# Kernel tuning notes

Hardware: AMD Instinct MI355X
Metric: run time of the kernel (lower is better)

Reference implementation:

```python
import jax, jax.numpy as jnp
import numpy as np

REL_DIM = 1024
NUM_HEADS = 16
HEAD_DIM = REL_DIM // NUM_HEADS
REL_EMB_DIM = 256
B, K = 32, 512
SCALE = 1.0 / float(np.sqrt(HEAD_DIM))


def setup_inputs() -> dict:
    key = jax.random.key(0)
    ks = jax.random.split(key, 7)
    s = 1.0 / float(np.sqrt(REL_DIM))
    return {
        "h_R": jax.random.normal(ks[0], (B, K, REL_DIM), dtype=jnp.float32),
        "R": jax.random.normal(ks[1], (K, REL_EMB_DIM), dtype=jnp.float32),
        "W_q": jax.random.normal(ks[2], (REL_DIM, REL_DIM), dtype=jnp.float32) * s,
        "W_k": jax.random.normal(ks[3], (REL_DIM, REL_DIM), dtype=jnp.float32) * s,
        "W_v": jax.random.normal(ks[4], (REL_DIM, REL_DIM), dtype=jnp.float32) * s,
        "W_o": jax.random.normal(ks[5], (REL_DIM, REL_DIM), dtype=jnp.float32) * s,
        "w_sim": jax.random.normal(ks[6], (NUM_HEADS,), dtype=jnp.float32) * 0.1,
    }


def reference(h_R, R, W_q, W_k, W_v, W_o, w_sim):
    Bb, Kk, _ = h_R.shape
    H, D = NUM_HEADS, HEAD_DIM
    # torch Linear: x @ W.T ; then split heads -> (B, H, K, D)
    def proj(x, W):
        return jnp.einsum('bkd,ed->bke', x, W).reshape(Bb, Kk, H, D).transpose(0, 2, 1, 3)
    q = proj(h_R, W_q)
    k = proj(h_R, W_k)
    v = proj(h_R, W_v)
    attn = jnp.einsum('bhqd,bhkd->bhqk', q, k) * SCALE
    # cosine-similarity bias (batch-independent): (H, K, K)
    R_norm = R / jnp.maximum(jnp.linalg.norm(R, axis=-1, keepdims=True), 1e-12)
    sim = R_norm @ R_norm.T  # (K, K)
    bias = w_sim[:, None, None] * sim[None]  # (H, K, K)
    attn = attn + bias[None]
    alpha = jax.nn.softmax(attn, axis=-1)
    out = jnp.einsum('bhqk,bhkd->bhqd', alpha, v)
    out = out.transpose(0, 2, 1, 3).reshape(Bb, Kk, H * D)
    return jnp.einsum('bkd,ed->bke', out, W_o)
```

## Files before the change

kernel.cpp:

```cpp
#include <hip/hip_runtime.h>

#define SEQK 512
#define NH 16
#define HD 64
#define RD 1024
#define BBATCH 32
#define QK_SCALE 0.125f
#define LOG2E 1.4426950408889634f

typedef unsigned short u16;
typedef unsigned int u32;
using bf16x8 = __attribute__((ext_vector_type(8))) short;
using f32x4  = __attribute__((ext_vector_type(4))) float;
using f32x16 = __attribute__((ext_vector_type(16))) float;

__device__ __forceinline__ u16 f2bf(float f) {
  unsigned u = __float_as_uint(f);
  u += 0x7FFFu + ((u >> 16) & 1u);
  return (u16)(u >> 16);
}
__device__ __forceinline__ float bf2f(u16 v) {
  return __uint_as_float(((unsigned)v) << 16);
}
__device__ __forceinline__ float fexp2(float x) {
  float r;
  asm("v_exp_f32 %0, %1" : "=v"(r) : "v"(x));
  return r;
}
__device__ __forceinline__ u32 pkbf(float lo, float hi) {
  u32 r;
  asm("v_cvt_pk_bf16_f32 %0, %1, %2" : "=v"(r) : "v"(lo), "v"(hi));
  return r;
}
__device__ __forceinline__ void plswap(u32& a, u32& b) {
#if __has_builtin(__builtin_amdgcn_permlane32_swap)
  typedef int v2i __attribute__((ext_vector_type(2)));
  v2i r = __builtin_amdgcn_permlane32_swap((int)a, (int)b, false, false);
  a = (u32)r[0]; b = (u32)r[1];
#else
  asm volatile("v_permlane32_swap_b32 %0, %1" : "+v"(a), "+v"(b));
#endif
}

__device__ __forceinline__ void async_cp16(const void* g, void* l) {
  __builtin_amdgcn_global_load_lds(
      (__attribute__((address_space(1))) void*)(void*)g,
      (__attribute__((address_space(3))) void*)l,
      16, 0, 0);
}

__global__ void convert_kernel(const float* __restrict__ hR,
                               const float* __restrict__ Wq, const float* __restrict__ Wk,
                               const float* __restrict__ Wv, const float* __restrict__ Wo,
                               u16* __restrict__ hR16,
                               u16* __restrict__ Wq16, u16* __restrict__ Wk16,
                               u16* __restrict__ Wv16, u16* __restrict__ Wo16) {
  size_t i4 = (size_t)blockIdx.x * blockDim.x + threadIdx.x;
  size_t e = i4 * 4;
  const float* src; u16* dst; size_t off;
  if (e < 16777216u) { src = hR; dst = hR16; off = e; }
  else {
    size_t r = e - 16777216u;
    int w = (int)(r >> 20);
    off = r & 1048575u;
    src = (w == 0 ? Wq : w == 1 ? Wk : w == 2 ? Wv : Wo);
    dst = (w == 0 ? Wq16 : w == 1 ? Wk16 : w == 2 ? Wv16 : Wo16);
  }
  float4 v = *(const float4*)(src + off);
  ushort4 o;
  o.x = f2bf(v.x); o.y = f2bf(v.y); o.z = f2bf(v.z); o.w = f2bf(v.w);
  *(ushort4*)(dst + off) = o;
}

__global__ void rnorm_kernel(const float* __restrict__ R, float* __restrict__ Rn) {
  int row = blockIdx.x;
  int lane = threadIdx.x;
  float4 v = *(const float4*)(R + (size_t)row * 256 + lane * 4);
  float ss = v.x * v.x + v.y * v.y + v.z * v.z + v.w * v.w;
  for (int off = 32; off; off >>= 1) ss += __shfl_xor(ss, off);
  float s = 1.0f / fmaxf(sqrtf(ss), 1e-12f);
  float4 o = {v.x * s, v.y * s, v.z * s, v.w * s};
  *(float4*)(Rn + (size_t)row * 256 + lane * 4) = o;
}

__global__ void sim_kernel(const float* __restrict__ Rn, u16* __restrict__ sim16) {
  __shared__ float Rl[16 * 256];
  int i0 = blockIdx.x * 16;
  int t = threadIdx.x;
  #pragma unroll
  for (int i = 0; i < 4; i++) {
    int f = t + i * 256;
    *(float4*)&Rl[f * 4] = *(const float4*)(Rn + (size_t)i0 * 256 + f * 4);
  }
  __syncthreads();
  for (int jj = 0; jj < 2; jj++) {
    int j = jj * 256 + t;
    float acc[16];
    #pragma unroll
    for (int i = 0; i < 16; i++) acc[i] = 0.f;
    for (int c = 0; c < 64; c++) {
      float4 rv = *(const float4*)(Rn + (size_t)j * 256 + c * 4);
      #pragma unroll
      for (int i = 0; i < 16; i++) {
        float4 a = *(const float4*)&Rl[i * 256 + c * 4];
        acc[i] += a.x * rv.x + a.y * rv.y + a.z * rv.z + a.w * rv.w;
      }
    }
    #pragma unroll
    for (int i = 0; i < 16; i++) sim16[(size_t)(i0 + i) * 512 + j] = f2bf(acc[i]);
  }
}

template <int MODE>
__global__ __launch_bounds__(256)
void gemm_kernel(const u16* __restrict__ A,
                 const u16* __restrict__ B0, const u16* __restrict__ B1,
                 const u16* __restrict__ B2,
                 u16* __restrict__ q16, u16* __restrict__ k16, u16* __restrict__ v16,
                 float* __restrict__ outF) {
  __shared__ u16 Alds[128 * 32];
  __shared__ u16 Blds[128 * 32];
  int tid = threadIdx.x;
  int wave = tid >> 6, lane = tid & 63;
  int wm = wave & 1, wn = wave >> 1;
  int lr = lane & 15, qd = lane >> 4;
  int mb = blockIdx.x * 128;
  int ny = blockIdx.y;

  const u16* Bmat;
  int nbmat;
  if (MODE == 0) {
    int wsel = ny >> 3;
    Bmat = (wsel == 0 ? B0 : wsel == 1 ? B1 : B2);
    nbmat = (ny & 7) * 128;
  } else {
    Bmat = B0;
    nbmat = ny * 128;
  }

  f32x4 zero = {0.f, 0.f, 0.f, 0.f};
  f32x4 acc[4][4];
  #pragma unroll
  for (int i = 0; i < 4; i++)
    #pragma unroll
    for (int j = 0; j < 4; j++) acc[i][j] = zero;

  for (int kb = 0; kb < 1024; kb += 32) {
    #pragma unroll
    for (int j = 0; j < 2; j++) {
      int r = (wave * 2 + j) * 16 + (lane >> 2);
      int c = (lane & 3) ^ ((r >> 1) & 3);
      async_cp16(A + (size_t)(mb + r) * 1024 + kb + c * 8,
                 &Alds[(wave * 2 + j) * 512]);
      async_cp16(Bmat + (size_t)(nbmat + r) * 1024 + kb + c * 8,
                 &Blds[(wave * 2 + j) * 512]);
    }
    __syncthreads();

    bf16x8 af[4], bf[4];
    #pragma unroll
    for (int mi = 0; mi < 4; mi++) {
      int ra = wm * 64 + mi * 16 + lr;
      af[mi] = *(const bf16x8*)&Alds[ra * 32 + ((qd ^ ((ra >> 1) & 3)) << 3)];
      int rb = wn * 64 + mi * 16 + lr;
      bf[mi] = *(const bf16x8*)&Blds[rb * 32 + ((qd ^ ((rb >> 1) & 3)) << 3)];
    }
    #pragma unroll
    for (int mi = 0; mi < 4; mi++)
      #pragma unroll
      for (int ni = 0; ni < 4; ni++)
        acc[mi][ni] = __builtin_amdgcn_mfma_f32_16x16x32_bf16(af[mi], bf[ni],
                                                              acc[mi][ni], 0, 0, 0);
    __syncthreads();
  }

  if (MODE == 0) {
    int wsel = ny >> 3;
    u16* dst = (wsel == 0 ? q16 : wsel == 1 ? k16 : v16);
    float scl = (wsel == 0) ? QK_SCALE * LOG2E : 1.0f;
    #pragma unroll
    for (int mi = 0; mi < 4; mi++) {
      int m = mb + wm * 64 + mi * 16 + qd * 4;
      int b = m >> 9, kk = m & 511;
      #pragma unroll
      for (int ni = 0; ni < 4; ni++) {
        int n = nbmat + wn * 64 + ni * 16 + lr;
        int h = n >> 6, d = n & 63;
        u16* p = dst + ((size_t)(b * 16 + h) * 512 + kk) * 64 + d;
        #pragma unroll
        for (int r = 0; r < 4; r++) p[(size_t)r * 64] = f2bf(acc[mi][ni][r] * scl);
      }
    }
  } else {
    #pragma unroll
    for (int mi = 0; mi < 4; mi++) {
      int m = mb + wm * 64 + mi * 16 + qd * 4;
      #pragma unroll
      for (int ni = 0; ni < 4; ni++) {
        int n = ny * 128 + wn * 64 + ni * 16 + lr;
        #pragma unroll
        for (int r = 0; r < 4; r++) outF[(size_t)(m + r) * 1024 + n] = acc[mi][ni][r];
      }
    }
  }
}

__global__ void vtrans_kernel(const u16* __restrict__ v16, u16* __restrict__ vt16) {
  __shared__ u16 tile[64 * 72];
  int kt = blockIdx.x;
  int bh = blockIdx.y;
  int t = threadIdx.x;
  const u16* src = v16 + ((size_t)bh * 512 + kt * 64) * 64;
  #pragma unroll
  for (int j = 0; j < 2; j++) {
    int linear = j * 2048 + t * 8;
    int kr = linear >> 6, d0 = linear & 63;
    bf16x8 vv = *(const bf16x8*)(src + (size_t)kr * 64 + d0);
    #pragma unroll
    for (int e = 0; e < 8; e++) tile[kr * 72 + d0 + e] = (u16)vv[e];
  }
  __syncthreads();
  #pragma unroll
  for (int j = 0; j < 2; j++) {
    int linear = j * 2048 + t * 8;
    int dr = linear >> 6, k0 = linear & 63;
    bf16x8 ov;
    #pragma unroll
    for (int e = 0; e < 8; e++) ov[e] = (short)tile[(k0 + e) * 72 + dr];
    *(bf16x8*)(vt16 + ((size_t)bh * 64 + dr) * 512 + kt * 64 + k0) = ov;
  }
}

__global__ __launch_bounds__(256, 3)
void attn_kernel(const u16* __restrict__ q16, const u16* __restrict__ k16,
                 const u16* __restrict__ vt16, const u16* __restrict__ sim16,
                 const float* __restrict__ wsim, u16* __restrict__ attn16) {
  __shared__ u16 smem[16384];

  int id = blockIdx.x;
  int xcd = id & 7;
  int j = id >> 3;
  int qt = j & 3;
  int bh = xcd * 64 + (j >> 2);
  int b = bh >> 4, h = bh & 15;

  int tid = threadIdx.x;
  int wave = tid >> 6, lane = tid & 63;
  int l31 = lane & 31, hi = lane >> 5;
  int qb = qt * 128 + wave * 32;

  const u16* qp = q16 + ((size_t)bh * 512 + qb + l31) * 64 + hi * 8;
  bf16x8 aq[4];
  #pragma unroll
  for (int ds = 0; ds < 4; ds++) aq[ds] = *(const bf16x8*)(qp + ds * 16);

  float ws = wsim[h] * LOG2E;

  f32x16 o[2];
  #pragma unroll
  for (int dt = 0; dt < 2; dt++)
    #pragma unroll
    for (int r = 0; r < 16; r++) o[dt][r] = 0.f;
  float m_run = -1e30f, l_run = 0.f;

  const u16* kbase = k16 + (size_t)bh * 512 * 64;
  const u16* vbase = vt16 + (size_t)bh * 64 * 512;

  auto stage = [&](int nb, int ck) {
    int k0 = ck * 64;
    u16* kd = smem + nb * 4096;
    u16* vd = smem + 8192 + nb * 4096;
    #pragma unroll
    for (int it = 0; it < 2; it++) {
      int idx = it * 256 + wave * 64 + lane;
      int r = idx >> 3, c8 = idx & 7;
      async_cp16(kbase + (size_t)(k0 + r) * 64 + ((c8 ^ (r & 7)) << 3),
                 kd + (it * 256 + wave * 64) * 8);
    }
    #pragma unroll
    for (int it = 0; it < 2; it++) {
      int idx = it * 256 + wave * 64 + lane;
      int dr = idx >> 3, c8 = idx & 7;
      async_cp16(vbase + (size_t)dr * 512 + k0 + ((c8 ^ (dr & 7)) << 3),
                 vd + (it * 256 + wave * 64) * 8);
    }
  };

  stage(0, 0);
  __syncthreads();

  int cur = 0;
  for (int ck = 0; ck < 8; ck++) {
    int k0 = ck * 64;

    uint2 braw[8];
    #pragma unroll
    for (int kb = 0; kb < 2; kb++)
      #pragma unroll
      for (int g = 0; g < 4; g++)
        braw[kb * 4 + g] = *(const uint2*)(sim16 + (size_t)(qb + l31) * 512 +
                                           k0 + kb * 32 + g * 8 + hi * 4);
    __builtin_amdgcn_sched_barrier(0);
    if (ck < 7) stage(cur ^ 1, ck + 1);

    const u16* Kc = smem + cur * 4096;
    const u16* Vc = smem + 8192 + cur * 4096;

    f32x16 s[2];
    __builtin_amdgcn_s_setprio(1);
    #pragma unroll
    for (int kb = 0; kb < 2; kb++) {
      f32x16 acc;
      #pragma unroll
      for (int r = 0; r < 16; r++) {
        u32 w = ((r >> 1) & 1) ? braw[kb * 4 + (r >> 2)].y
                               : braw[kb * 4 + (r >> 2)].x;
        acc[r] = ws * __uint_as_float((r & 1) ? (w & 0xFFFF0000u) : (w << 16));
      }
      int koff = kb * 32 + l31;
      #pragma unroll
      for (int ds = 0; ds < 4; ds++) {
        bf16x8 kf = *(const bf16x8*)&Kc[koff * 64 + (((ds * 2 + hi) ^ (koff & 7)) << 3)];
        acc = __builtin_amdgcn_mfma_f32_32x32x16_bf16(kf, aq[ds], acc, 0, 0, 0);
      }
      s[kb] = acc;
    }
    __builtin_amdgcn_s_setprio(0);

    float v8[8];
    #pragma unroll
    for (int i = 0; i < 8; i++)
      v8[i] = fmaxf(fmaxf(s[0][i], s[0][i + 8]), fmaxf(s[1][i], s[1][i + 8]));
    float m_in = fmaxf(fmaxf(fmaxf(v8[0], v8[1]), fmaxf(v8[2], v8[3])),
                       fmaxf(fmaxf(v8[4], v8[5]), fmaxf(v8[6], v8[7])));
    u32 xa = __float_as_uint(m_in), xb = __float_as_uint(m_in);
    plswap(xa, xb);
    float m_tile = fmaxf(__uint_as_float(xa), __uint_as_float(xb));
    float mnew = fmaxf(m_run, m_tile);
    float alpha = fexp2(m_run - mnew);
    m_run = mnew;

    float c0 = 0.f, c1 = 0.f, c2 = 0.f, c3 = 0.f;
    #pragma unroll
    for (int kb = 0; kb < 2; kb++)
      #pragma unroll
      for (int i = 0; i < 16; i++) {
        float e = fexp2(s[kb][i] - mnew);
        s[kb][i] = e;
        if ((i & 3) == 0) c0 += e; else if ((i & 3) == 1) c1 += e;
        else if ((i & 3) == 2) c2 += e; else c3 += e;
      }
    float cs = (c0 + c1) + (c2 + c3);
    u32 ya = __float_as_uint(cs), yb = __float_as_uint(cs);
    plswap(ya, yb);
    float cs_tot = __uint_as_float(ya) + __uint_as_float(yb);
    l_run = l_run * alpha + cs_tot;

    #pragma unroll
    for (int dt = 0; dt < 2; dt++) o[dt] *= alpha;

    __builtin_amdgcn_s_setprio(1);
    #pragma unroll
    for (int ks = 0; ks < 4; ks++) {
      int kb = ks >> 1, j4 = (ks & 1) * 8;
      u32 a0 = pkbf(s[kb][j4 + 0], s[kb][j4 + 1]);
      u32 a1 = pkbf(s[kb][j4 + 2], s[kb][j4 + 3]);
      u32 b0 = pkbf(s[kb][j4 + 4], s[kb][j4 + 5]);
      u32 b1 = pkbf(s[kb][j4 + 6], s[kb][j4 + 7]);
      plswap(a0, b0);
      plswap(a1, b1);
      union { u32 w[4]; bf16x8 v; } U;
      U.w[0] = a0; U.w[1] = a1; U.w[2] = b0; U.w[3] = b1;
      #pragma unroll
      for (int dt = 0; dt < 2; dt++) {
        int dr = dt * 32 + l31;
        bf16x8 vf = *(const bf16x8*)&Vc[dr * 64 + (((ks * 2 + hi) ^ (dr & 7)) << 3)];
        o[dt] = __builtin_amdgcn_mfma_f32_32x32x16_bf16(vf, U.v, o[dt], 0, 0, 0);
      }
    }
    __builtin_amdgcn_s_setprio(0);

    __syncthreads();
    cur ^= 1;
  }

  float linv = 1.0f / l_run;
  u16* Ow = smem + wave * 2304;
  #pragma unroll
  for (int dt = 0; dt < 2; dt++)
    #pragma unroll
    for (int g = 0; g < 4; g++) {
      u32 w0 = pkbf(o[dt][4 * g + 0] * linv, o[dt][4 * g + 1] * linv);
      u32 w1 = pkbf(o[dt][4 * g + 2] * linv, o[dt][4 * g + 3] * linv);
      uint2 pr; pr.x = w0; pr.y = w1;
      *(uint2*)&Ow[l31 * 72 + dt * 32 + g * 8 + hi * 4] = pr;
    }
  #pragma unroll
  for (int i = 0; i < 4; i++) {
    int idx = i * 64 + lane;
    int row = idx >> 3, seg = idx & 7;
    bf16x8 val = *(const bf16x8*)&Ow[row * 72 + seg * 8];
    *(bf16x8*)(attn16 + ((size_t)b * 512 + qb + row) * 1024 + h * 64 + seg * 8) = val;
  }
}

extern "C" void kernel_launch(void* const* d_in, const int* in_sizes, int n_in,
                              void* d_out, int out_size, void* d_ws, size_t ws_size,
                              hipStream_t stream) {
  const float* hR  = (const float*)d_in[0];
  const float* R   = (const float*)d_in[1];
  const float* Wq  = (const float*)d_in[2];
  const float* Wk  = (const float*)d_in[3];
  const float* Wv  = (const float*)d_in[4];
  const float* Wo  = (const float*)d_in[5];
  const float* wsm = (const float*)d_in[6];
  float* out = (float*)d_out;

  const size_t NE = 16777216;
  u16* ws16   = (u16*)d_ws;
  u16* hR16   = ws16;
  u16* attn16 = ws16;
  u16* q16    = ws16 + NE;
  u16* k16    = ws16 + 2 * NE;
  u16* v16    = ws16 + 3 * NE;
  u16* vt16   = ws16 + 4 * NE;
  u16* Wq16   = ws16 + 5 * NE;
  u16* Wk16   = Wq16 + 1048576;
  u16* Wv16   = Wk16 + 1048576;
  u16* Wo16   = Wv16 + 1048576;
  u16* sim16  = Wo16 + 1048576;
  float* Rn   = (float*)(sim16 + 262144);

  convert_kernel<<<20480, 256, 0, stream>>>(hR, Wq, Wk, Wv, Wo,
                                            hR16, Wq16, Wk16, Wv16, Wo16);
  rnorm_kernel<<<512, 64, 0, stream>>>(R, Rn);
  sim_kernel<<<32, 256, 0, stream>>>(Rn, sim16);
  gemm_kernel<0><<<dim3(128, 24), 256, 0, stream>>>(hR16, Wq16, Wk16, Wv16,
                                                    q16, k16, v16, nullptr);
  vtrans_kernel<<<dim3(8, 512), 256, 0, stream>>>(v16, vt16);
  attn_kernel<<<2048, 256, 0, stream>>>(q16, k16, vt16, sim16, wsm, attn16);
  gemm_kernel<1><<<dim3(128, 8), 256, 0, stream>>>(attn16, Wo16, nullptr, nullptr,
                                                   nullptr, nullptr, nullptr, out);
}
```

Measured before the change: 454.4 us.

## Rewrite projection GEMMs as 256x256-tile, 8-wave, double-buffered pipelined kernel

```diff
diff --git a/kernel.cpp b/kernel.cpp
--- a/kernel.cpp
+++ b/kernel.cpp
@@ -111,80 +111,144 @@
   }
 }
 
+#define GEMM_PHASE(AB, BB, MH, NH, STAGE, WAITSTMT) {                         \
+    bf16x8 af[4][2], bfv[2][2];                                               \
+    _Pragma("unroll") for (int mi2 = 0; mi2 < 4; mi2++) {                     \
+      int r = wm * 128 + ((MH) * 4 + mi2) * 16 + lr;                          \
+      int sw = ((r >> 2) & 1) << 1;                                           \
+      _Pragma("unroll") for (int ks = 0; ks < 2; ks++)                        \
+        af[mi2][ks] = *(const bf16x8*)&(AB)[r * 64 + ((ks * 4 + qd) ^ sw) * 8]; \
+    }                                                                         \
+    _Pragma("unroll") for (int ni2 = 0; ni2 < 2; ni2++) {                     \
+      int r = wn * 64 + ((NH) * 2 + ni2) * 16 + lr;                           \
+      int sw = ((r >> 2) & 1) << 1;                                           \
+      _Pragma("unroll") for (int ks = 0; ks < 2; ks++)                        \
+        bfv[ni2][ks] = *(const bf16x8*)&(BB)[r * 64 + ((ks * 4 + qd) ^ sw) * 8]; \
+    }                                                                         \
+    STAGE;                                                                    \
+    __builtin_amdgcn_sched_barrier(0);                                        \
+    __builtin_amdgcn_s_barrier();                                             \
+    __builtin_amdgcn_sched_barrier(0);                                        \
+    __builtin_amdgcn_s_setprio(1);                                            \
+    _Pragma("unroll") for (int mi2 = 0; mi2 < 4; mi2++)                       \
+      _Pragma("unroll") for (int ni2 = 0; ni2 < 2; ni2++)                     \
+        _Pragma("unroll") for (int ks = 0; ks < 2; ks++)                      \
+          acc[(MH) * 4 + mi2][(NH) * 2 + ni2] =                               \
+              __builtin_amdgcn_mfma_f32_16x16x32_bf16(                        \
+                  af[mi2][ks], bfv[ni2][ks],                                  \
+                  acc[(MH) * 4 + mi2][(NH) * 2 + ni2], 0, 0, 0);              \
+    __builtin_amdgcn_s_setprio(0);                                            \
+    WAITSTMT;                                                                 \
+    __builtin_amdgcn_sched_barrier(0);                                        \
+    __builtin_amdgcn_s_barrier();                                             \
+  }
+
 template <int MODE>
-__global__ __launch_bounds__(256)
+__global__ __launch_bounds__(512, 2)
 void gemm_kernel(const u16* __restrict__ A,
                  const u16* __restrict__ B0, const u16* __restrict__ B1,
                  const u16* __restrict__ B2,
                  u16* __restrict__ q16, u16* __restrict__ k16, u16* __restrict__ v16,
                  float* __restrict__ outF) {
-  __shared__ u16 Alds[128 * 32];
-  __shared__ u16 Blds[128 * 32];
+  __shared__ u16 smem[65536];
+  u16* const As0 = smem;
+  u16* const As1 = smem + 16384;
+  u16* const Bs0 = smem + 32768;
+  u16* const Bs1 = smem + 49152;
+
   int tid = threadIdx.x;
   int wave = tid >> 6, lane = tid & 63;
-  int wm = wave & 1, wn = wave >> 1;
+  int wm = wave >> 2, wn = wave & 3;
   int lr = lane & 15, qd = lane >> 4;
-  int mb = blockIdx.x * 128;
+  int mb = blockIdx.x * 256;
   int ny = blockIdx.y;
 
   const u16* Bmat;
-  int nbmat;
+  int nbase;
   if (MODE == 0) {
-    int wsel = ny >> 3;
+    int wsel = ny >> 2;
     Bmat = (wsel == 0 ? B0 : wsel == 1 ? B1 : B2);
-    nbmat = (ny & 7) * 128;
+    nbase = (ny & 3) * 256;
   } else {
     Bmat = B0;
-    nbmat = ny * 128;
-  }
-
-  f32x4 zero = {0.f, 0.f, 0.f, 0.f};
-  f32x4 acc[4][4];
-  #pragma unroll
-  for (int i = 0; i < 4; i++)
-    #pragma unroll
-    for (int j = 0; j < 4; j++) acc[i][j] = zero;
-
-  for (int kb = 0; kb < 1024; kb += 32) {
-    #pragma unroll
-    for (int j = 0; j < 2; j++) {
-      int r = (wave * 2 + j) * 16 + (lane >> 2);
-      int c = (lane & 3) ^ ((r >> 1) & 3);
-      async_cp16(A + (size_t)(mb + r) * 1024 + kb + c * 8,
-                 &Alds[(wave * 2 + j) * 512]);
-      async_cp16(Bmat + (size_t)(nbmat + r) * 1024 + kb + c * 8,
-                 &Blds[(wave * 2 + j) * 512]);
-    }
-    __syncthreads();
-
-    bf16x8 af[4], bf[4];
-    #pragma unroll
-    for (int mi = 0; mi < 4; mi++) {
-      int ra = wm * 64 + mi * 16 + lr;
-      af[mi] = *(const bf16x8*)&Alds[ra * 32 + ((qd ^ ((ra >> 1) & 3)) << 3)];
-      int rb = wn * 64 + mi * 16 + lr;
-      bf[mi] = *(const bf16x8*)&Blds[rb * 32 + ((qd ^ ((rb >> 1) & 3)) << 3)];
-    }
-    #pragma unroll
-    for (int mi = 0; mi < 4; mi++)
-      #pragma unroll
-      for (int ni = 0; ni < 4; ni++)
-        acc[mi][ni] = __builtin_amdgcn_mfma_f32_16x16x32_bf16(af[mi], bf[ni],
-                                                              acc[mi][ni], 0, 0, 0);
-    __syncthreads();
+    nbase = ny * 256;
+  }
+  const u16* Ag = A + (size_t)mb * 1024;
+  const u16* Bg = Bmat + (size_t)nbase * 1024;
+
+  auto stageA_ = [&](u16* dst, const u16* gsrc, int half) {
+    int blk = ((wave < 4) ? 0 : 2) + half;
+    int ws = wave & 3;
+    #pragma unroll
+    for (int jj = 0; jj < 2; jj++) {
+      int rbase = blk * 64 + ws * 16 + jj * 8;
+      int row = rbase + (lane >> 3);
+      int c8 = (lane & 7) ^ (((row >> 2) & 1) << 1);
+      async_cp16(gsrc + (size_t)row * 1024 + c8 * 8, dst + rbase * 64);
+    }
+  };
+  auto stageB_ = [&](u16* dst, const u16* gsrc, int half) {
+    int st = wave >> 1, sub = wave & 1;
+    #pragma unroll
+    for (int jj = 0; jj < 2; jj++) {
+      int rbase = st * 64 + half * 32 + sub * 16 + jj * 8;
+      int row = rbase + (lane >> 3);
+      int c8 = (lane & 7) ^ (((row >> 2) & 1) << 1);
+      async_cp16(gsrc + (size_t)row * 1024 + c8 * 8, dst + rbase * 64);
+    }
+  };
+
+  f32x4 acc[8][4];
+  #pragma unroll
+  for (int i = 0; i < 8; i++)
+    #pragma unroll
+    for (int j = 0; j < 4; j++) acc[i][j] = f32x4{0.f, 0.f, 0.f, 0.f};
+
+  stageA_(As0, Ag, 0);
+  stageB_(Bs0, Bg, 0);
+  stageA_(As0, Ag, 1);
+  stageB_(Bs0, Bg, 1);
+  stageA_(As1, Ag + 64, 0);
+  stageB_(Bs1, Bg + 64, 0);
+  asm volatile("s_waitcnt vmcnt(4)" ::: "memory");
+  __builtin_amdgcn_sched_barrier(0);
+  __builtin_amdgcn_s_barrier();
+
+  #pragma unroll 1
+  for (int i = 0; i < 8; i++) {
+    int t1 = 2 * i + 1;
+    bool more = (i < 7);
+    const u16* Ag1 = Ag + t1 * 64;
+    const u16* Bg1 = Bg + t1 * 64;
+    const u16* Ag2 = Ag + (t1 + 1) * 64;
+    const u16* Bg2 = Bg + (t1 + 1) * 64;
+    const u16* Ag3 = Ag + (t1 + 2) * 64;
+    const u16* Bg3 = Bg + (t1 + 2) * 64;
+
+    GEMM_PHASE(As0, Bs0, 0, 0, { stageA_(As1, Ag1, 1); }, {});
+    GEMM_PHASE(As0, Bs0, 0, 1, { stageB_(Bs1, Bg1, 1); }, {});
+    GEMM_PHASE(As0, Bs0, 1, 0, { if (more) stageA_(As0, Ag2, 0); }, {});
+    GEMM_PHASE(As0, Bs0, 1, 1, { if (more) stageB_(Bs0, Bg2, 0); },
+               { if (more) asm volatile("s_waitcnt vmcnt(4)" ::: "memory");
+                 else      asm volatile("s_waitcnt vmcnt(0)" ::: "memory"); });
+    GEMM_PHASE(As1, Bs1, 0, 0, { if (more) stageA_(As0, Ag2, 1); }, {});
+    GEMM_PHASE(As1, Bs1, 0, 1, { if (more) stageB_(Bs0, Bg2, 1); }, {});
+    GEMM_PHASE(As1, Bs1, 1, 0, { if (more) stageA_(As1, Ag3, 0); }, {});
+    GEMM_PHASE(As1, Bs1, 1, 1, { if (more) stageB_(Bs1, Bg3, 0); },
+               { if (more) asm volatile("s_waitcnt vmcnt(4)" ::: "memory"); });
   }
 
   if (MODE == 0) {
-    int wsel = ny >> 3;
+    int wsel = ny >> 2;
     u16* dst = (wsel == 0 ? q16 : wsel == 1 ? k16 : v16);
     float scl = (wsel == 0) ? QK_SCALE * LOG2E : 1.0f;
     #pragma unroll
-    for (int mi = 0; mi < 4; mi++) {
-      int m = mb + wm * 64 + mi * 16 + qd * 4;
+    for (int mi = 0; mi < 8; mi++) {
+      int m = mb + wm * 128 + mi * 16 + qd * 4;
       int b = m >> 9, kk = m & 511;
       #pragma unroll
       for (int ni = 0; ni < 4; ni++) {
-        int n = nbmat + wn * 64 + ni * 16 + lr;
+        int n = nbase + wn * 64 + ni * 16 + lr;
         int h = n >> 6, d = n & 63;
         u16* p = dst + ((size_t)(b * 16 + h) * 512 + kk) * 64 + d;
         #pragma unroll
@@ -193,11 +257,11 @@
     }
   } else {
     #pragma unroll
-    for (int mi = 0; mi < 4; mi++) {
-      int m = mb + wm * 64 + mi * 16 + qd * 4;
+    for (int mi = 0; mi < 8; mi++) {
+      int m = mb + wm * 128 + mi * 16 + qd * 4;
       #pragma unroll
       for (int ni = 0; ni < 4; ni++) {
-        int n = ny * 128 + wn * 64 + ni * 16 + lr;
+        int n = nbase + wn * 64 + ni * 16 + lr;
         #pragma unroll
         for (int r = 0; r < 4; r++) outF[(size_t)(m + r) * 1024 + n] = acc[mi][ni][r];
       }
@@ -435,10 +499,10 @@
                                             hR16, Wq16, Wk16, Wv16, Wo16);
   rnorm_kernel<<<512, 64, 0, stream>>>(R, Rn);
   sim_kernel<<<32, 256, 0, stream>>>(Rn, sim16);
-  gemm_kernel<0><<<dim3(128, 24), 256, 0, stream>>>(hR16, Wq16, Wk16, Wv16,
-                                                    q16, k16, v16, nullptr);
+  gemm_kernel<0><<<dim3(64, 12), 512, 0, stream>>>(hR16, Wq16, Wk16, Wv16,
+                                                   q16, k16, v16, nullptr);
   vtrans_kernel<<<dim3(8, 512), 256, 0, stream>>>(v16, vt16);
   attn_kernel<<<2048, 256, 0, stream>>>(q16, k16, vt16, sim16, wsm, attn16);
-  gemm_kernel<1><<<dim3(128, 8), 256, 0, stream>>>(attn16, Wo16, nullptr, nullptr,
-                                                   nullptr, nullptr, nullptr, out);
-}
+  gemm_kernel<1><<<dim3(64, 4), 512, 0, stream>>>(attn16, Wo16, nullptr, nullptr,
+                                                  nullptr, nullptr, nullptr, out);
+}
```

Measured after the change: 463.9 us. 2.1% more time.
